# Kernel optimization log

Hardware: AMD Instinct MI355X
Metric: run time of the kernel (lower is better)

## Reference

```python
import jax, jax.numpy as jnp
import numpy as np
from jax import lax

G, K, C_IN, C_FEAT, H, W, B = 8, 6, 512, 256, 64, 64, 1


def apply_offset(offset):
    # offset: [N, 2, H, W] pixel-space offsets -> sampling grid [N, H, W, 2] in [-1, 1]
    # channel 0 displaces x (width), channel 1 displaces y (height), matching the
    # reversed-meshgrid logic of the original torch apply_offset.
    n, _, h, w = offset.shape
    jj = jnp.arange(w, dtype=offset.dtype)[None, None, :]
    ii = jnp.arange(h, dtype=offset.dtype)[None, :, None]
    gx = (jj + offset[:, 0]) / ((w - 1.0) / 2.0) - 1.0
    gy = (ii + offset[:, 1]) / ((h - 1.0) / 2.0) - 1.0
    return jnp.stack([gx, gy], axis=-1)


def grid_sample_border(img, grid):
    # img: [N, C, H, W], grid: [N, H, W, 2] in [-1, 1]
    # Bilinear, padding_mode='border', align_corners=False (torch grid_sample default).
    n, c, h, w = img.shape
    x = jnp.clip((grid[..., 0] + 1.0) * w * 0.5 - 0.5, 0.0, w - 1.0)
    y = jnp.clip((grid[..., 1] + 1.0) * h * 0.5 - 0.5, 0.0, h - 1.0)
    x0 = jnp.floor(x)
    y0 = jnp.floor(y)
    wx = (x - x0)[:, None]  # [N,1,H,W]
    wy = (y - y0)[:, None]
    x0i = x0.astype(jnp.int32)
    y0i = y0.astype(jnp.int32)
    x1i = jnp.minimum(x0i + 1, w - 1)
    y1i = jnp.minimum(y0i + 1, h - 1)

    def gather(im, yi, xi):  # im [C,H,W]; yi, xi [H,W]
        return im[:, yi, xi]

    g = jax.vmap(gather)
    v00 = g(img, y0i, x0i)
    v01 = g(img, y0i, x1i)
    v10 = g(img, y1i, x0i)
    v11 = g(img, y1i, x1i)
    return (1.0 - wy) * ((1.0 - wx) * v00 + wx * v01) + wy * ((1.0 - wx) * v10 + wx * v11)


def setup_inputs() -> dict:
    key = jax.random.key(0)
    ks = jax.random.split(key, 11)
    s = 0.02
    return {
        "gar_feat": jax.random.normal(ks[0], (B, C_FEAT, H, W), jnp.float32),
        "cond_feat": jax.random.normal(ks[1], (B, C_FEAT, H, W), jnp.float32),
        "mask": jax.random.uniform(ks[2], (B, G, C_FEAT), dtype=jnp.float32),
        "W1": jax.random.normal(ks[3], (G, 128, C_IN, 3, 3), jnp.float32) * s,
        "b1": jax.random.normal(ks[4], (G, 128), jnp.float32) * s,
        "W2": jax.random.normal(ks[5], (G, 64, 128, 3, 3), jnp.float32) * s,
        "b2": jax.random.normal(ks[6], (G, 64), jnp.float32) * s,
        "W3": jax.random.normal(ks[7], (G, 32, 64, 3, 3), jnp.float32) * s,
        "b3": jax.random.normal(ks[8], (G, 32), jnp.float32) * s,
        "W4": jax.random.normal(ks[9], (G, 3 * K, 32, 3, 3), jnp.float32) * s,
        "b4": jax.random.normal(ks[10], (G, 3 * K), jnp.float32) * s,
    }


def reference(gar_feat, cond_feat, mask, W1, b1, W2, b2, W3, b3, W4, b4):
    b, c, h, w = gar_feat.shape
    g = W1.shape[0]
    k = W4.shape[1] // 3
    inp = jnp.concatenate([gar_feat, cond_feat], axis=1)  # [B, 2C, H, W]

    def conv(x, wgt, bias):
        return lax.conv_general_dilated(
            x, wgt, (1, 1), 'SAME', dimension_numbers=('NCHW', 'OIHW', 'NCHW')
        ) + bias[None, :, None, None]

    def lrelu(x):
        return jnp.where(x >= 0, x, 0.1 * x)

    def group_net(w1, bb1, w2, bb2, w3, bb3, w4, bb4):
        hid = lrelu(conv(inp, w1, bb1))
        hid = lrelu(conv(hid, w2, bb2))
        hid = lrelu(conv(hid, w3, bb3))
        return conv(hid, w4, bb4)  # [B, 3k, H, W]

    oa = jax.vmap(group_net)(W1, b1, W2, b2, W3, b3, W4, b4)  # [G, B, 3k, H, W]
    attn = jax.nn.softmax(oa[:, :, 2 * k:], axis=0)           # softmax across groups: [G,B,k,H,W]
    off = oa[:, :, :2 * k].reshape(g, b * k, 2, h, w)
    grid = jax.vmap(apply_offset)(off)                        # [G, B*k, H, W, 2]

    rep = jnp.repeat(gar_feat, k, axis=0)                     # [B*k, C, H, W]

    def warp_group(grid_g, attn_g, mask_g):
        samp = grid_sample_border(rep, grid_g).reshape(b, k, c, h, w)
        wfeat = jnp.sum(samp * attn_g[:, :, None], axis=1)    # [B, C, H, W]
        return wfeat * mask_g[:, :, None, None]

    warped = jax.vmap(warp_group)(grid, attn, jnp.transpose(mask, (1, 0, 2)))
    return jnp.sum(warped, axis=0)  # [B, C, H, W]
```

## Files before the change

kernel.cpp:

```cpp
#include <hip/hip_runtime.h>
#include <hip/hip_bf16.h>

typedef __hip_bfloat16 bf16;
typedef unsigned short ushort8v __attribute__((ext_vector_type(8)));
typedef short  s16x4  __attribute__((ext_vector_type(4)));
typedef short  bf16x8 __attribute__((ext_vector_type(8)));
typedef float  f32x4  __attribute__((ext_vector_type(4)));

#define HW 4096
#define IMG_W 64

__device__ __forceinline__ float bfbits2f(unsigned short u) {
    return __uint_as_float(((unsigned int)u) << 16);
}
__device__ __forceinline__ short f2bs(float f) {
    bf16 h = __float2bfloat16(f);
    return *reinterpret_cast<short*>(&h);
}

__device__ __forceinline__ void gl_lds16(const void* g, void* s) {
    __builtin_amdgcn_global_load_lds(
        (const __attribute__((address_space(1))) unsigned int*)g,
        (__attribute__((address_space(3))) unsigned int*)s, 16, 0, 0);
}

__device__ void pack_input_dev(const float* __restrict__ gar,
                               const float* __restrict__ cond,
                               short* __restrict__ outp, int bx2, float* tile)
{
    int bx = bx2 & 127;
    int by = bx2 >> 7;
    int tx = threadIdx.x & 31;
    int ty = threadIdx.x >> 5;
#pragma unroll
    for (int i = 0; i < 4; ++i) {
        int c = by * 32 + ty + i * 8;
        const float* src = (c < 256) ? (gar + (size_t)c * HW)
                                     : (cond + (size_t)(c - 256) * HW);
        tile[(ty + i * 8) * 33 + tx] = src[bx * 32 + tx];
    }
    __syncthreads();
#pragma unroll
    for (int i = 0; i < 4; ++i) {
        int p = bx * 32 + ty + i * 8;
        outp[((size_t)by * 4096 + p) * 32 + tx] = f2bs(tile[tx * 33 + ty + i * 8]);
    }
}

template<int CIN, int CREAL, int BN, int NT, bool COAL>
__device__ void pack_w_dev(const float* __restrict__ wgt, char* __restrict__ wp,
                           int bx, short* sT)
{
    constexpr int NCC  = CIN / 32;
    constexpr int BLKB = 9 * 4 * BN * 16;

    const int t  = threadIdx.x;
    const int cc = bx % NCC;
    const int nt = (bx / NCC) % NT;
    const int g  = bx / (NT * NCC);

    for (int i = t; i < BLKB / 8; i += 256)
        reinterpret_cast<s16x4*>(sT)[i] = s16x4{0, 0, 0, 0};
    __syncthreads();

    int ocmax = CREAL - nt * BN; if (ocmax > BN) ocmax = BN;
    const size_t base = ((size_t)(g * CREAL + nt * BN) * CIN + cc * 32) * 9;
    for (int i = t; i < ocmax * 288; i += 256) {
        int oc = i / 288;
        int r  = i % 288;
        int ic = r / 9, tap = r % 9;
        size_t idx;
        if (COAL) idx = (size_t)(((tap * BN + oc) * 4 + (ic >> 3)) * 8 + (ic & 7));
        else      idx = (size_t)(((tap * 4 + (ic >> 3)) * BN + oc) * 8 + (ic & 7));
        sT[idx] = f2bs(wgt[base + (size_t)oc * CIN * 9 + r]);
    }
    __syncthreads();

    const s16x4* src = reinterpret_cast<const s16x4*>(sT);
    s16x4* dst = reinterpret_cast<s16x4*>(wp + (size_t)bx * BLKB);
    for (int i = t; i < BLKB / 8; i += 256)
        dst[i] = src[i];
}

__global__ __launch_bounds__(256)
void pack_all(const float* __restrict__ gar, const float* __restrict__ cond,
              const float* __restrict__ W1, const float* __restrict__ W2,
              const float* __restrict__ W3, const float* __restrict__ W4,
              short* inp_t, char* W1p, char* W2p, char* W3p, char* W4p)
{
    __shared__ __align__(16) short sbuf[9 * 4 * 64 * 8];
    int bx = blockIdx.x;
    if (bx < 256)      pack_w_dev<512, 128, 64, 2, true >(W1, W1p, bx,       sbuf);
    else if (bx < 288) pack_w_dev<128,  64, 64, 1, false>(W2, W2p, bx - 256, sbuf);
    else if (bx < 304) pack_w_dev< 64,  32, 32, 1, false>(W3, W3p, bx - 288, sbuf);
    else if (bx < 312) pack_w_dev< 32,  18, 32, 1, false>(W4, W4p, bx - 304, sbuf);
    else pack_input_dev(gar, cond, inp_t, bx - 312, (float*)sbuf);
}

template<int ICP, int CREAL, int BN, int ROWS, int OF, int NT, int NW, int PIPE,
         bool PIXMAJ_OUT, bool LEAKY, bool OUT_F32>
__global__ __launch_bounds__(NW * 64, 2)
void conv_mfma(const short* __restrict__ inp, const char* __restrict__ wp,
               const float* __restrict__ bias, void* __restrict__ outv)
{
    constexpr int NCC  = ICP / 32;
    constexpr int HALO = ROWS + 2;
    constexpr int NPT  = 4096 / (ROWS * 64);
    constexpr int BLKB = 9 * 4 * BN * 16;
    constexpr int RNDS = BLKB / 1024;
    constexpr int NBUF = (PIPE && NCC > 1) ? 2 : 1;
    constexpr int SMAX = (HALO + NW - 1) / NW;

    __shared__ __align__(16) short sA[HALO][4][68][8];
    __shared__ __align__(16) char  sBraw[NBUF][BLKB];

    const int b  = blockIdx.x;
    const int g  = b & 7;
    const int r_ = b >> 3;
    const int pt = r_ % NPT;
    const int nt = r_ / NPT;
    const int r0 = pt * ROWS;

    const int t    = threadIdx.x;
    const int wave = t >> 6, lane = t & 63;
    const int l15  = lane & 15, quad = lane >> 4;

    int row_l, ocw;
    if (NW == 8) {
        if (ROWS == 4) { row_l = wave >> 1; ocw = (wave & 1) * (BN / 2); }
        else           { row_l = wave >> 2; ocw = (wave & 3) * (BN / 4); }
    } else {
        row_l = (ROWS == 4) ? wave : (wave & 1);
        ocw   = (ROWS == 4) ? 0 : (wave >> 1) * (BN / 2);
    }

    const size_t gpix = (ICP == 512) ? 0 : ((size_t)g * 4096);
    const char*  wb   = wp + (size_t)((g * NT + nt) * NCC) * BLKB;

    const int acol = t & 63;
    const int r2   = t >> 6;

    bf16x8 pre[SMAX][4];

    auto stageA_load = [&](int cc) {
#pragma unroll
        for (int s = 0; s < SMAX; ++s) {
            int j = r2 + s * NW;
            if (j < HALO) {
                int gy = r0 - 1 + j;
                if (gy >= 0 && gy < 64) {
                    const short* sp = inp + ((gpix + gy * 64 + acol) * ICP + cc * 32);
#pragma unroll
                    for (int q = 0; q < 4; ++q)
                        pre[s][q] = *reinterpret_cast<const bf16x8*>(sp + q * 8);
                } else {
#pragma unroll
                    for (int q = 0; q < 4; ++q)
                        pre[s][q] = bf16x8{0, 0, 0, 0, 0, 0, 0, 0};
                }
            }
        }
    };
    auto stageA_write = [&]() {
#pragma unroll
        for (int s = 0; s < SMAX; ++s) {
            int j = r2 + s * NW;
            if (j < HALO) {
#pragma unroll
                for (int q = 0; q < 4; ++q)
                    *reinterpret_cast<bf16x8*>(&sA[j][q][acol + 1][0]) = pre[s][q];
            }
        }
    };
    auto stageB = [&](int cc) {
        const char* wsrc = wb + (size_t)cc * BLKB;
        char* sbb = (char*)sBraw[(NBUF == 2) ? (cc & 1) : 0];
        for (int r = wave; r < RNDS; r += NW)
            gl_lds16(wsrc + r * 1024 + lane * 16, sbb + r * 1024);
    };

    f32x4 acc[OF][4];
#pragma unroll
    for (int o = 0; o < OF; ++o)
#pragma unroll
        for (int p = 0; p < 4; ++p)
#pragma unroll
            for (int r = 0; r < 4; ++r) acc[o][p][r] = 0.f;

    if (t < HALO * 8) {
        int row = t >> 3, q = (t >> 1) & 3, cp = (t & 1) ? 65 : 0;
        *reinterpret_cast<bf16x8*>(&sA[row][q][cp][0]) =
            bf16x8{0, 0, 0, 0, 0, 0, 0, 0};
    }

    stageB(0);
    stageA_load(0);
    stageA_write();

    for (int cc = 0; cc < NCC; ++cc) {
        __syncthreads();
        if (cc + 1 < NCC) {
            if (PIPE) stageB(cc + 1);
            stageA_load(cc + 1);
        }
        const bf16x8* sBv = reinterpret_cast<const bf16x8*>(
            sBraw[(NBUF == 2) ? (cc & 1) : 0]);

#pragma unroll
        for (int dy = 0; dy < 3; ++dy) {
#pragma unroll
            for (int dx = 0; dx < 3; ++dx) {
                bf16x8 pF[4];
#pragma unroll
                for (int p = 0; p < 4; ++p)
                    pF[p] = *reinterpret_cast<const bf16x8*>(
                        &sA[row_l + dy][quad][p * 16 + l15 + dx][0]);
                bf16x8 wF[OF];
#pragma unroll
                for (int o = 0; o < OF; ++o)
                    wF[o] = sBv[((dy * 3 + dx) * 4 + quad) * BN + ocw + o * 16 + l15];
#pragma unroll
                for (int o = 0; o < OF; ++o)
#pragma unroll
                    for (int p = 0; p < 4; ++p)
                        acc[o][p] = __builtin_amdgcn_mfma_f32_16x16x32_bf16(
                            wF[o], pF[p], acc[o][p], 0, 0, 0);
            }
        }
        __syncthreads();
        if (cc + 1 < NCC) {
            if (!PIPE) stageB(cc + 1);
            stageA_write();
        }
    }

    const int prow = r0 + row_l;
#pragma unroll
    for (int o = 0; o < OF; ++o)
#pragma unroll
        for (int reg = 0; reg < 4; ++reg) {
            const int ocl = ocw + o * 16 + quad * 4 + reg;
            const int ocg = nt * BN + ocl;
            if (ocg < CREAL) {
                const float bv = bias[g * CREAL + ocg];
                if (PIXMAJ_OUT) {
                    short* outp = (short*)outv;
                    const size_t pixbase = ((size_t)g * 4096 + prow * 64);
#pragma unroll
                    for (int p = 0; p < 4; ++p) {
                        float v = acc[o][p][reg] + bv;
                        if (LEAKY) v = v >= 0.f ? v : 0.1f * v;
                        outp[(pixbase + p * 16 + l15) * (NT * BN) + ocg] = f2bs(v);
                    }
                } else if (OUT_F32) {
                    float* outp = (float*)outv;
                    const size_t base = ((size_t)(g * CREAL + ocg)) * HW + prow * IMG_W;
#pragma unroll
                    for (int p = 0; p < 4; ++p) {
                        float v = acc[o][p][reg] + bv;
                        if (LEAKY) v = v >= 0.f ? v : 0.1f * v;
                        outp[base + p * 16 + l15] = v;
                    }
                } else {
                    short* outp = (short*)outv;
                    const size_t base = ((size_t)(g * CREAL + ocg)) * HW + prow * IMG_W;
#pragma unroll
                    for (int p = 0; p < 4; ++p) {
                        float v = acc[o][p][reg] + bv;
                        if (LEAKY) v = v >= 0.f ? v : 0.1f * v;
                        outp[base + p * 16 + l15] = f2bs(v);
                    }
                }
            }
        }
}

__global__ __launch_bounds__(256, 2)
void conv1_direct(const short* __restrict__ inp, const char* __restrict__ wp,
                  const float* __restrict__ bias, short* __restrict__ outp)
{
    __shared__ __align__(16) short sA[2][4][66][4][8];

    const int b  = blockIdx.x;
    const int g  = b & 7;
    const int r_ = b >> 3;
    const int pt = r_ & 31;
    const int nt = r_ >> 5;
    const int r0 = pt * 2;

    const int t    = threadIdx.x;
    const int wave = t >> 6, lane = t & 63;
    const int l15  = lane & 15, quad = lane >> 4;

    const int row_l = wave & 1;
    const int ocw   = (wave >> 1) * 32;

    const short* wb    = (const short*)wp + (size_t)(g * 2 + nt) * 16 * 18432;
    const short* wlane = wb + ((size_t)(ocw + l15) * 4 + quad) * 8;

    auto stageDMA = [&](int cc, int buf) {
        int gy = r0 - 1 + wave;
        if (gy >= 0 && gy < 64) {
            const short* src = inp + ((size_t)cc * 4096 + (size_t)gy * 64) * 32
                                   + (size_t)lane * 8;
#pragma unroll
            for (int c4 = 0; c4 < 4; ++c4)
                gl_lds16(src + c4 * 512, &sA[buf][wave][1 + c4 * 16][0][0]);
        }
    };

    bf16x8 wA[9][2], wB[9][2];
    auto loadW_into = [&](int cc, bf16x8 (&w)[9][2]) {
        const short* ws = wlane + (size_t)cc * 18432;
#pragma unroll
        for (int tap = 0; tap < 9; ++tap)
#pragma unroll
            for (int o = 0; o < 2; ++o)
                w[tap][o] = *reinterpret_cast<const bf16x8*>(
                    ws + tap * 2048 + o * 512);
    };

    f32x4 acc[2][4];
#pragma unroll
    for (int o = 0; o < 2; ++o)
#pragma unroll
        for (int p = 0; p < 4; ++p)
#pragma unroll
            for (int r = 0; r < 4; ++r) acc[o][p][r] = 0.f;

    loadW_into(0, wA);
    stageDMA(0, 0);
    if (t < 64) {
        int buf = t >> 5, row = (t >> 3) & 3, q = (t >> 1) & 3;
        int col = (t & 1) ? 65 : 0;
        *reinterpret_cast<bf16x8*>(&sA[buf][row][col][q][0]) =
            bf16x8{0, 0, 0, 0, 0, 0, 0, 0};
    }
    if (r0 == 0 || r0 == 62) {
        int zr = (r0 == 0) ? 0 : 3;
        for (int i = t; i < 2 * 66 * 4; i += 256) {
            int buf = i / 264, rem = i % 264;
            *reinterpret_cast<bf16x8*>(&sA[buf][zr][rem >> 2][rem & 3][0]) =
                bf16x8{0, 0, 0, 0, 0, 0, 0, 0};
        }
    }

    auto body = [&](int cc, int cur, bf16x8 (&wuse)[9][2], bf16x8 (&wld)[9][2]) {
        __syncthreads();
        if (cc + 1 < 16) {
            stageDMA(cc + 1, cur ^ 1);
            loadW_into(cc + 1, wld);
        }
#pragma unroll
        for (int dy = 0; dy < 3; ++dy)
#pragma unroll
            for (int dx = 0; dx < 3; ++dx) {
                bf16x8 pF[4];
#pragma unroll
                for (int p = 0; p < 4; ++p)
                    pF[p] = *reinterpret_cast<const bf16x8*>(
                        &sA[cur][row_l + dy][p * 16 + l15 + dx][quad][0]);
#pragma unroll
                for (int o = 0; o < 2; ++o)
#pragma unroll
                    for (int p = 0; p < 4; ++p)
                        acc[o][p] = __builtin_amdgcn_mfma_f32_16x16x32_bf16(
                            wuse[dy * 3 + dx][o], pF[p], acc[o][p], 0, 0, 0);
            }
    };

    for (int c2 = 0; c2 < 16; c2 += 2) {
        body(c2,     0, wA, wB);
        body(c2 + 1, 1, wB, wA);
    }

    const int prow = r0 + row_l;
    const size_t pixbase = (size_t)g * 4096 + (size_t)prow * 64;
#pragma unroll
    for (int o = 0; o < 2; ++o)
#pragma unroll
        for (int reg = 0; reg < 4; ++reg) {
            const int ocg = nt * 64 + ocw + o * 16 + quad * 4 + reg;
            const float bv = bias[g * 128 + ocg];
#pragma unroll
            for (int p = 0; p < 4; ++p) {
                float v = acc[o][p][reg] + bv;
                v = v >= 0.f ? v : 0.1f * v;
                outp[(pixbase + p * 16 + l15) * 128 + ocg] = f2bs(v);
            }
        }
}

__global__ __launch_bounds__(256, 4)
void conv1_ks(const short* __restrict__ inp, const char* __restrict__ wp,
              float* __restrict__ part0, float* __restrict__ part1)
{
    __shared__ __align__(16) short sA[2][4][66][4][8];

    const int b  = blockIdx.x;
    const int g  = b & 7;
    const int r_ = b >> 3;
    const int pt = r_ & 31;
    const int nt = (r_ >> 5) & 1;
    const int ks = r_ >> 6;
    const int r0 = pt * 2;
    const int cc0 = ks * 8;

    const int t    = threadIdx.x;
    const int wave = t >> 6, lane = t & 63;
    const int l15  = lane & 15, quad = lane >> 4;

    const int row_l = wave & 1;
    const int ocw   = (wave >> 1) * 32;

    const short* wb    = (const short*)wp + (size_t)(g * 2 + nt) * 16 * 18432;
    const short* wlane = wb + ((size_t)(ocw + l15) * 4 + quad) * 8;

    auto stageDMA = [&](int cc, int buf) {
        int gy = r0 - 1 + wave;
        if (gy >= 0 && gy < 64) {
            const short* src = inp + ((size_t)cc * 4096 + (size_t)gy * 64) * 32
                                   + (size_t)lane * 8;
#pragma unroll
            for (int c4 = 0; c4 < 4; ++c4)
                gl_lds16(src + c4 * 512, &sA[buf][wave][1 + c4 * 16][0][0]);
        }
    };

    f32x4 acc[2][4];
#pragma unroll
    for (int o = 0; o < 2; ++o)
#pragma unroll
        for (int p = 0; p < 4; ++p)
#pragma unroll
            for (int r = 0; r < 4; ++r) acc[o][p][r] = 0.f;

    stageDMA(cc0, 0);
    if (t < 64) {
        int buf = t >> 5, row = (t >> 3) & 3, q = (t >> 1) & 3;
        int col = (t & 1) ? 65 : 0;
        *reinterpret_cast<bf16x8*>(&sA[buf][row][col][q][0]) =
            bf16x8{0, 0, 0, 0, 0, 0, 0, 0};
    }
    if (r0 == 0 || r0 == 62) {
        int zr = (r0 == 0) ? 0 : 3;
        for (int i = t; i < 2 * 66 * 4; i += 256) {
            int buf = i / 264, rem = i % 264;
            *reinterpret_cast<bf16x8*>(&sA[buf][zr][rem >> 2][rem & 3][0]) =
                bf16x8{0, 0, 0, 0, 0, 0, 0, 0};
        }
    }

    auto body = [&](int i, int cur) {
        const int cc = cc0 + i;
        __syncthreads();
        if (i + 1 < 8) stageDMA(cc + 1, cur ^ 1);
        const short* wcc = wlane + (size_t)cc * 18432;
#pragma unroll
        for (int dy = 0; dy < 3; ++dy)
#pragma unroll
            for (int dx = 0; dx < 3; ++dx) {
                bf16x8 pF[4];
#pragma unroll
                for (int p = 0; p < 4; ++p)
                    pF[p] = *reinterpret_cast<const bf16x8*>(
                        &sA[cur][row_l + dy][p * 16 + l15 + dx][quad][0]);
                bf16x8 w0 = *reinterpret_cast<const bf16x8*>(
                    wcc + (dy * 3 + dx) * 2048);
                bf16x8 w1 = *reinterpret_cast<const bf16x8*>(
                    wcc + (dy * 3 + dx) * 2048 + 512);
#pragma unroll
                for (int p = 0; p < 4; ++p)
                    acc[0][p] = __builtin_amdgcn_mfma_f32_16x16x32_bf16(
                        w0, pF[p], acc[0][p], 0, 0, 0);
#pragma unroll
                for (int p = 0; p < 4; ++p)
                    acc[1][p] = __builtin_amdgcn_mfma_f32_16x16x32_bf16(
                        w1, pF[p], acc[1][p], 0, 0, 0);
            }
    };

    for (int i2 = 0; i2 < 8; i2 += 2) {
        body(i2,     0);
        body(i2 + 1, 1);
    }

    float* pp = ks ? part1 : part0;
    const int prow = r0 + row_l;
    const size_t pixbase = (size_t)g * 4096 + (size_t)prow * 64;
#pragma unroll
    for (int o = 0; o < 2; ++o)
#pragma unroll
        for (int reg = 0; reg < 4; ++reg) {
            const int ocg = nt * 64 + ocw + o * 16 + quad * 4 + reg;
#pragma unroll
            for (int p = 0; p < 4; ++p)
                pp[(pixbase + p * 16 + l15) * 128 + ocg] = acc[o][p][reg];
        }
}

__global__ __launch_bounds__(256)
void finalize_conv1(const float* __restrict__ p0, const float* __restrict__ p1,
                    const float* __restrict__ bias, short* __restrict__ outp)
{
    const size_t i8 = ((size_t)blockIdx.x * 256 + threadIdx.x) * 8;
    const int oc0 = (int)(i8 & 127);
    const int g   = (int)(i8 >> 19);
    float4 a0 = *reinterpret_cast<const float4*>(p0 + i8);
    float4 a1 = *reinterpret_cast<const float4*>(p0 + i8 + 4);
    float4 b0 = *reinterpret_cast<const float4*>(p1 + i8);
    float4 b1 = *reinterpret_cast<const float4*>(p1 + i8 + 4);
    float4 c0 = *reinterpret_cast<const float4*>(bias + g * 128 + oc0);
    float4 c1 = *reinterpret_cast<const float4*>(bias + g * 128 + oc0 + 4);
    float v[8] = {a0.x + b0.x + c0.x, a0.y + b0.y + c0.y,
                  a0.z + b0.z + c0.z, a0.w + b0.w + c0.w,
                  a1.x + b1.x + c1.x, a1.y + b1.y + c1.y,
                  a1.z + b1.z + c1.z, a1.w + b1.w + c1.w};
    ushort8v r;
#pragma unroll
    for (int j = 0; j < 8; ++j) {
        float x = v[j] >= 0.f ? v[j] : 0.1f * v[j];
        r[j] = (unsigned short)f2bs(x);
    }
    *reinterpret_cast<ushort8v*>(outp + i8) = r;
}

__global__ __launch_bounds__(256)
void warp_combine_kernel(const float* __restrict__ oa,
                         const short* __restrict__ inp_t,
                         const float* __restrict__ mask,
                         float* __restrict__ out)
{
    __shared__ __align__(16) float4 sWts[8][6][8];
    __shared__ __align__(16) int4   sIdx[8][6][8];

    const int t = threadIdx.x;

    if (t < 48) {
        int lp = t / 6;
        int k  = t % 6;
        int p  = blockIdx.x * 8 + lp;
        int x  = p & 63, y = p >> 6;

        float l[8];
        float m = -1e30f;
#pragma unroll
        for (int g = 0; g < 8; ++g) {
            l[g] = oa[(size_t)(g * 18 + 12 + k) * HW + p];
            m = fmaxf(m, l[g]);
        }
        float s = 0.f;
#pragma unroll
        for (int g = 0; g < 8; ++g) { l[g] = __expf(l[g] - m); s += l[g]; }
        float inv = 1.f / s;

#pragma unroll
        for (int g = 0; g < 8; ++g) {
            float a  = l[g] * inv;
            float ox = oa[(size_t)(g * 18 + 2 * k)     * HW + p];
            float oy = oa[(size_t)(g * 18 + 2 * k + 1) * HW + p];
            float sx = fminf(fmaxf(((float)x + ox) * (64.f / 63.f) - 0.5f, 0.f), 63.f);
            float sy = fminf(fmaxf(((float)y + oy) * (64.f / 63.f) - 0.5f, 0.f), 63.f);
            float fx0 = floorf(sx), fy0 = floorf(sy);
            int   x0 = (int)fx0,    y0i = (int)fy0;
            float wx = sx - fx0,    wy = sy - fy0;
            int   x1 = min(x0 + 1, 63), y1 = min(y0i + 1, 63);
            sWts[lp][k][g] = make_float4(a * (1.f - wy) * (1.f - wx),
                                         a * (1.f - wy) * wx,
                                         a * wy * (1.f - wx),
                                         a * wy * wx);
            sIdx[lp][k][g] = make_int4(y0i * 64 + x0, y0i * 64 + x1,
                                       y1  * 64 + x0, y1  * 64 + x1);
        }
    }
    __syncthreads();

    const int lp = t >> 5;
    const int p  = blockIdx.x * 8 + lp;
    const int c0 = (t & 31) * 8;
    const short* ipc = inp_t + (size_t)(c0 >> 5) * (4096 * 32) + (c0 & 31);

    float acc[8];
#pragma unroll
    for (int j = 0; j < 8; ++j) acc[j] = 0.f;

    for (int g = 0; g < 8; ++g) {
        float4 m0 = *reinterpret_cast<const float4*>(mask + g * 256 + c0);
        float4 m1 = *reinterpret_cast<const float4*>(mask + g * 256 + c0 + 4);
        float mk[8] = {m0.x, m0.y, m0.z, m0.w, m1.x, m1.y, m1.z, m1.w};
#pragma unroll
        for (int k = 0; k < 6; ++k) {
            float4 w  = sWts[lp][k][g];
            int4   id = sIdx[lp][k][g];
            ushort8v v00 = *reinterpret_cast<const ushort8v*>(ipc + (size_t)id.x * 32);
            ushort8v v01 = *reinterpret_cast<const ushort8v*>(ipc + (size_t)id.y * 32);
            ushort8v v10 = *reinterpret_cast<const ushort8v*>(ipc + (size_t)id.z * 32);
            ushort8v v11 = *reinterpret_cast<const ushort8v*>(ipc + (size_t)id.w * 32);
#pragma unroll
            for (int j = 0; j < 8; ++j) {
                float sv = w.x * bfbits2f(v00[j]) + w.y * bfbits2f(v01[j])
                         + w.z * bfbits2f(v10[j]) + w.w * bfbits2f(v11[j]);
                acc[j] = fmaf(mk[j], sv, acc[j]);
            }
        }
    }
#pragma unroll
    for (int j = 0; j < 8; ++j)
        out[(size_t)(c0 + j) * HW + p] = acc[j];
}

extern "C" void kernel_launch(void* const* d_in, const int* in_sizes, int n_in,
                              void* d_out, int out_size, void* d_ws, size_t ws_size,
                              hipStream_t stream)
{
    (void)in_sizes; (void)n_in; (void)out_size;
    const float* gar  = (const float*)d_in[0];
    const float* cond = (const float*)d_in[1];
    const float* mask = (const float*)d_in[2];
    const float* W1   = (const float*)d_in[3];
    const float* b1   = (const float*)d_in[4];
    const float* W2   = (const float*)d_in[5];
    const float* b2   = (const float*)d_in[6];
    const float* W3   = (const float*)d_in[7];
    const float* b3   = (const float*)d_in[8];
    const float* W4   = (const float*)d_in[9];
    const float* b4   = (const float*)d_in[10];
    float* out = (float*)d_out;

    char* ws = (char*)d_ws;
    short* inp_t  = (short*)(ws);
    char*  W1p    = ws + (4u << 20);
    short* hid2_t = (short*)(ws + (4u << 20));
    short* hid3_t = (short*)(ws + (8u << 20));
    float* oa     = (float*)(ws + (10u << 20) + (512u << 10));
    char*  W2p    = ws + (14u << 20);
    char*  W3p    = ws + (15u << 20) + (512u << 10);
    char*  W4p    = ws + (16u << 20);
    short* hid1_t = (short*)(ws + (17u << 20));
    float* part0  = (float*)(ws + (28u << 20));
    float* part1  = (float*)(ws + (44u << 20));

    pack_all<<<2360, 256, 0, stream>>>(gar, cond, W1, W2, W3, W4,
                                       inp_t, W1p, W2p, W3p, W4p);

    if (ws_size >= ((size_t)60 << 20)) {
        conv1_ks<<<1024, 256, 0, stream>>>(inp_t, W1p, part0, part1);
        finalize_conv1<<<2048, 256, 0, stream>>>(part0, part1, b1, hid1_t);
    } else {
        conv1_direct<<<512, 256, 0, stream>>>(inp_t, W1p, b1, hid1_t);
    }
    conv_mfma<128, 64, 64, 2, 1, 1, 8, 1, true, true, false>
        <<<256, 512, 0, stream>>>(hid1_t, W2p, b2, hid2_t);
    conv_mfma<64, 32, 32, 2, 1, 1, 4, 1, true, true, false>
        <<<256, 256, 0, stream>>>(hid2_t, W3p, b3, hid3_t);
    conv_mfma<32, 18, 32, 2, 1, 1, 4, 1, false, false, true>
        <<<256, 256, 0, stream>>>(hid3_t, W4p, b4, oa);

    warp_combine_kernel<<<512, 256, 0, stream>>>(oa, inp_t, mask, out);
}
```

Before: 206.3 us.

## Widen conv1 split-K tile to 64 output channels per wave, halving block count

The conv1 split-K kernel now has each wave compute 64 output channels (four 16-wide MFMA tiles) instead of 32. Each block covers all 128 channels, so every staged input row in LDS is reused across twice as many channels and the grid drops from 1024 to 512 blocks. All nine taps' weights for a channel chunk are loaded into registers before the MFMA loop. This doubles the accumulator and weight register footprint, so the occupancy hint falls from 4 to 2 waves per SIMD and spills or weaker latency hiding are possible.

```diff
diff --git a/kernel.cpp b/kernel.cpp
--- a/kernel.cpp
+++ b/kernel.cpp
@@ -391,9 +391,9 @@
         }
 }
 
-__global__ __launch_bounds__(256, 4)
-void conv1_ks(const short* __restrict__ inp, const char* __restrict__ wp,
-              float* __restrict__ part0, float* __restrict__ part1)
+__global__ __launch_bounds__(256, 2)
+void conv1_of4(const short* __restrict__ inp, const char* __restrict__ wp,
+               float* __restrict__ part0, float* __restrict__ part1)
 {
     __shared__ __align__(16) short sA[2][4][66][4][8];
 
@@ -401,8 +401,7 @@
     const int g  = b & 7;
     const int r_ = b >> 3;
     const int pt = r_ & 31;
-    const int nt = (r_ >> 5) & 1;
-    const int ks = r_ >> 6;
+    const int ks = (r_ >> 5) & 1;
     const int r0 = pt * 2;
     const int cc0 = ks * 8;
 
@@ -411,10 +410,10 @@
     const int l15  = lane & 15, quad = lane >> 4;
 
     const int row_l = wave & 1;
-    const int ocw   = (wave >> 1) * 32;
-
-    const short* wb    = (const short*)wp + (size_t)(g * 2 + nt) * 16 * 18432;
-    const short* wlane = wb + ((size_t)(ocw + l15) * 4 + quad) * 8;
+    const int ntw   = wave >> 1;
+
+    const short* wb    = (const short*)wp + (size_t)(g * 2 + ntw) * 16 * 18432;
+    const short* wlane = wb + ((size_t)l15 * 4 + quad) * 8;
 
     auto stageDMA = [&](int cc, int buf) {
         int gy = r0 - 1 + wave;
@@ -427,9 +426,9 @@
         }
     };
 
-    f32x4 acc[2][4];
-#pragma unroll
-    for (int o = 0; o < 2; ++o)
+    f32x4 acc[4][4];
+#pragma unroll
+    for (int o = 0; o < 4; ++o)
 #pragma unroll
         for (int p = 0; p < 4; ++p)
 #pragma unroll
@@ -456,6 +455,15 @@
         __syncthreads();
         if (i + 1 < 8) stageDMA(cc + 1, cur ^ 1);
         const short* wcc = wlane + (size_t)cc * 18432;
+
+        bf16x8 w[9][4];
+#pragma unroll
+        for (int tap = 0; tap < 9; ++tap)
+#pragma unroll
+            for (int o = 0; o < 4; ++o)
+                w[tap][o] = *reinterpret_cast<const bf16x8*>(
+                    wcc + tap * 2048 + o * 512);
+
 #pragma unroll
         for (int dy = 0; dy < 3; ++dy)
 #pragma unroll
@@ -465,18 +473,12 @@
                 for (int p = 0; p < 4; ++p)
                     pF[p] = *reinterpret_cast<const bf16x8*>(
                         &sA[cur][row_l + dy][p * 16 + l15 + dx][quad][0]);
-                bf16x8 w0 = *reinterpret_cast<const bf16x8*>(
-                    wcc + (dy * 3 + dx) * 2048);
-                bf16x8 w1 = *reinterpret_cast<const bf16x8*>(
-                    wcc + (dy * 3 + dx) * 2048 + 512);
-#pragma unroll
-                for (int p = 0; p < 4; ++p)
-                    acc[0][p] = __builtin_amdgcn_mfma_f32_16x16x32_bf16(
-                        w0, pF[p], acc[0][p], 0, 0, 0);
-#pragma unroll
-                for (int p = 0; p < 4; ++p)
-                    acc[1][p] = __builtin_amdgcn_mfma_f32_16x16x32_bf16(
-                        w1, pF[p], acc[1][p], 0, 0, 0);
+#pragma unroll
+                for (int o = 0; o < 4; ++o)
+#pragma unroll
+                    for (int p = 0; p < 4; ++p)
+                        acc[o][p] = __builtin_amdgcn_mfma_f32_16x16x32_bf16(
+                            w[dy * 3 + dx][o], pF[p], acc[o][p], 0, 0, 0);
             }
     };
 
@@ -489,10 +491,10 @@
     const int prow = r0 + row_l;
     const size_t pixbase = (size_t)g * 4096 + (size_t)prow * 64;
 #pragma unroll
-    for (int o = 0; o < 2; ++o)
+    for (int o = 0; o < 4; ++o)
 #pragma unroll
         for (int reg = 0; reg < 4; ++reg) {
-            const int ocg = nt * 64 + ocw + o * 16 + quad * 4 + reg;
+            const int ocg = ntw * 64 + o * 16 + quad * 4 + reg;
 #pragma unroll
             for (int p = 0; p < 4; ++p)
                 pp[(pixbase + p * 16 + l15) * 128 + ocg] = acc[o][p][reg];
@@ -644,7 +646,7 @@
                                        inp_t, W1p, W2p, W3p, W4p);
 
     if (ws_size >= ((size_t)60 << 20)) {
-        conv1_ks<<<1024, 256, 0, stream>>>(inp_t, W1p, part0, part1);
+        conv1_of4<<<512, 256, 0, stream>>>(inp_t, W1p, part0, part1);
         finalize_conv1<<<2048, 256, 0, stream>>>(part0, part1, b1, hid1_t);
     } else {
         conv1_direct<<<512, 256, 0, stream>>>(inp_t, W1p, b1, hid1_t);
```

After: 210.1 us. About the same (+1.9%).
